# Optimization experiments

Hardware: AMD Instinct MI355X
Metric: run time of the kernel (lower is better)

Reference implementation:

```python
import jax, jax.numpy as jnp
import numpy as np

B, N, E = 2, 2048, 1024
H = 16
D = E // H  # head_dim = 64
MLP = 4096
EPS = 1e-5


def _layernorm(x, g, b):
    mu = jnp.mean(x, axis=-1, keepdims=True)
    var = jnp.var(x, axis=-1, keepdims=True)
    return (x - mu) * jax.lax.rsqrt(var + EPS) * g + b


def setup_inputs() -> dict:
    key = jax.random.key(0)
    ks = jax.random.split(key, 12)
    s_e = 1.0 / np.sqrt(E)
    s_m = 1.0 / np.sqrt(MLP)
    return {
        "x": jax.random.normal(ks[0], (B, N, E), jnp.float32),
        "w_qkv": jax.random.uniform(ks[1], (E, 3 * E), jnp.float32, -s_e, s_e),
        "b_qkv": jax.random.uniform(ks[2], (3 * E,), jnp.float32, -s_e, s_e),
        "w_proj": jax.random.uniform(ks[3], (E, E), jnp.float32, -s_e, s_e),
        "b_proj": jax.random.uniform(ks[4], (E,), jnp.float32, -s_e, s_e),
        "g1": jnp.ones((E,), jnp.float32),
        "beta1": jnp.zeros((E,), jnp.float32),
        "g2": jnp.ones((E,), jnp.float32),
        "beta2": jnp.zeros((E,), jnp.float32),
        "w_fc1": jax.random.uniform(ks[5], (E, MLP), jnp.float32, -s_e, s_e),
        "b_fc1": jax.random.uniform(ks[6], (MLP,), jnp.float32, -s_e, s_e),
        "w_fc2": jax.random.uniform(ks[7], (MLP, E), jnp.float32, -s_m, s_m),
        "b_fc2": jax.random.uniform(ks[8], (E,), jnp.float32, -s_m, s_m),
    }


def reference(x, w_qkv, b_qkv, w_proj, b_proj, g1, beta1, g2, beta2,
              w_fc1, b_fc1, w_fc2, b_fc2):
    scale = D ** (-0.5)
    # --- attention block (pre-norm) ---
    h = _layernorm(x, g1, beta1)
    qkv = (h @ w_qkv + b_qkv).reshape(B, N, 3, H, D)
    q, k, v = (qkv[:, :, i].transpose(0, 2, 1, 3) for i in range(3))  # [B,H,N,D]
    scores = jnp.einsum("bhnd,bhmd->bhnm", q, k) * scale  # [B,H,N,N]
    attn = jax.nn.softmax(scores, axis=-1)
    out = jnp.einsum("bhnm,bhmd->bhnd", attn, v)
    out = out.transpose(0, 2, 1, 3).reshape(B, N, E)
    x = x + (out @ w_proj + b_proj)
    # --- MLP block (pre-norm, exact GELU as in torch default) ---
    h = _layernorm(x, g2, beta2)
    h = jax.nn.gelu(h @ w_fc1 + b_fc1, approximate=False) @ w_fc2 + b_fc2
    return x + h
```

## Files before the change

### kernel.cpp

```cpp
#include <hip/hip_runtime.h>
#include <hip/hip_bf16.h>
#include <cmath>


typedef __hip_bfloat16 bf16;
typedef __bf16 bf16x8 __attribute__((ext_vector_type(8)));
typedef __bf16 bf16x4v __attribute__((ext_vector_type(4)));
typedef float  f32x4  __attribute__((ext_vector_type(4)));

#define CB 2
#define CN 2048
#define CE 1024
#define CH 16
#define CD 64
#define CMLP 4096
#define CM (CB*CN)

#define PS2 72

#define QPRE 0.18033688011112042f
#if __has_builtin(__builtin_amdgcn_exp2f)
#define EXP2(s) __builtin_amdgcn_exp2f(s)
#else
#define EXP2(s) __expf((s)*0.69314718055994531f)
#endif

__device__ __forceinline__ float b2f(bf16 v){ return __bfloat162float(v); }
__device__ __forceinline__ bf16  f2b(float v){ return __float2bfloat16(v); }

__device__ __forceinline__ void gl_lds16(const void* g, void* l){
  __builtin_amdgcn_global_load_lds((__attribute__((address_space(1))) void*)g,
                                   (__attribute__((address_space(3))) void*)l,
                                   16, 0, 0);
}

#define FENCE asm volatile("" ::: "memory")
#define BAR   do{ FENCE; __builtin_amdgcn_s_barrier(); FENCE; }while(0)
#define VMW6  asm volatile("s_waitcnt vmcnt(6)" ::: "memory")
#define VMW0  asm volatile("s_waitcnt vmcnt(0)" ::: "memory")

__global__ __launch_bounds__(256) void prep_k(
  const float* __restrict__ i0, bf16* __restrict__ o0,
  const float* __restrict__ i1, bf16* __restrict__ o1,
  const float* __restrict__ i2, bf16* __restrict__ o2,
  const float* __restrict__ i3, bf16* __restrict__ o3,
  const float* __restrict__ x,  const float* __restrict__ g,
  const float* __restrict__ be, bf16* __restrict__ lnout)
{
  __shared__ float tile[32][33];
  __shared__ float red[8];
  __shared__ float mu_s, rs_s;
  int t = blockIdx.x;
  const int tid = threadIdx.x;
  if(t >= 12288){
    const int row = t - 12288;
    const float4 v4 = ((const float4*)(x + (size_t)row*CE))[tid];
    float v[4] = {v4.x, v4.y, v4.z, v4.w};
    float s=0.f, s2=0.f;
    #pragma unroll
    for(int i=0;i<4;i++){ s+=v[i]; s2+=v[i]*v[i]; }
    #pragma unroll
    for(int off=32; off>0; off>>=1){ s += __shfl_down(s,off); s2 += __shfl_down(s2,off); }
    const int wv=tid>>6, ln=tid&63;
    if(ln==0){ red[wv]=s; red[4+wv]=s2; }
    __syncthreads();
    if(tid==0){
      float S=red[0]+red[1]+red[2]+red[3], S2=red[4]+red[5]+red[6]+red[7];
      float mu=S/CE;
      mu_s=mu; rs_s=rsqrtf(S2/CE - mu*mu + 1e-5f);
    }
    __syncthreads();
    const float mu=mu_s, rs=rs_s;
    #pragma unroll
    for(int i=0;i<4;i++){
      int c=tid*4+i;
      lnout[(size_t)row*CE+c] = f2b((v[i]-mu)*rs*g[c] + be[c]);
    }
    return;
  }
  const float* in; bf16* out; int K, N, nx;
  if(t < 3072){            in=i0; out=o0; K=1024; N=3072; nx=96; }
  else if(t < 4096){ t-=3072; in=i1; out=o1; K=1024; N=1024; nx=32; }
  else if(t < 8192){ t-=4096; in=i2; out=o2; K=1024; N=4096; nx=128; }
  else {             t-=8192; in=i3; out=o3; K=4096; N=1024; nx=32; }
  const int n0 = (t%nx)*32, k0 = (t/nx)*32;
  const int tx = tid & 31;
  const int ty = tid >> 5;
  #pragma unroll
  for(int i=0;i<32;i+=8) tile[ty+i][tx] = in[(size_t)(k0+ty+i)*N + n0+tx];
  __syncthreads();
  #pragma unroll
  for(int i=0;i<32;i+=8) out[(size_t)(n0+ty+i)*K + k0+tx] = f2b(tile[tx][ty+i]);
}

__global__ __launch_bounds__(256) void ln_k(const float* __restrict__ x,
                                            const float* __restrict__ g,
                                            const float* __restrict__ be,
                                            bf16* __restrict__ out){
  const int row = blockIdx.x;
  const int t = threadIdx.x;
  const float4 v4 = ((const float4*)(x + (size_t)row*CE))[t];
  float v[4] = {v4.x, v4.y, v4.z, v4.w};
  float s=0.f, s2=0.f;
  #pragma unroll
  for(int i=0;i<4;i++){ s+=v[i]; s2+=v[i]*v[i]; }
  #pragma unroll
  for(int off=32; off>0; off>>=1){ s += __shfl_down(s,off); s2 += __shfl_down(s2,off); }
  __shared__ float red[8];
  __shared__ float mu_s, rs_s;
  const int wv=t>>6, ln=t&63;
  if(ln==0){ red[wv]=s; red[4+wv]=s2; }
  __syncthreads();
  if(t==0){
    float S=red[0]+red[1]+red[2]+red[3], S2=red[4]+red[5]+red[6]+red[7];
    float mu=S/CE;
    mu_s=mu; rs_s=rsqrtf(S2/CE - mu*mu + 1e-5f);
  }
  __syncthreads();
  const float mu=mu_s, rs=rs_s;
  #pragma unroll
  for(int i=0;i<4;i++){
    int c=t*4+i;
    out[(size_t)row*CE+c] = f2b((v[i]-mu)*rs*g[c] + be[c]);
  }
}

#define EP_QKV 0
#define EP_RES 1
#define EP_GELU 2

template<int MODE, int BN>
__global__ __launch_bounds__(256,2) void gemm_k(
  const bf16* __restrict__ A, const bf16* __restrict__ BT,
  const float* __restrict__ bias, const float* __restrict__ res,
  float* __restrict__ Cf, bf16* __restrict__ Cb,
  bf16* __restrict__ Cq, bf16* __restrict__ Ck, bf16* __restrict__ Cv,
  int Ksz, int Nsz)
{
  constexpr int NJ = BN/32;
  constexpr int NBUF = (BN==64) ? 3 : 2;
  __shared__ __align__(16) bf16 Alds[NBUF][128*64];
  __shared__ __align__(16) bf16 Blds[NBUF][BN*64];
  const int tid = threadIdx.x;
  const int wave = tid>>6, lane = tid&63;
  const int m16 = lane&15, quad = lane>>4;
  const int wi = wave>>1, wj = wave&1;

  const int lin = blockIdx.x + gridDim.x*blockIdx.y;
  const int m_idx = (lin&7) + 8*((lin>>3)&3);
  const int n_idx = lin>>5;
  const size_t m0 = (size_t)m_idx*128;
  const size_t n0 = (size_t)n_idx*BN;

  f32x4 acc[4][NJ] = {};

  const int srow8 = lane>>3;
  const int schk  = ((lane&7)^srow8)*8;
  const bf16* pA = A  + (m0 + 32*wave      + srow8)*(size_t)Ksz + schk;
  const bf16* pB = BT + (n0 + (BN/4)*wave  + srow8)*(size_t)Ksz + schk;

  auto stage = [&](int buf, const bf16* gA, const bf16* gB){
    bf16* lA = &Alds[buf][wave*2048];
    bf16* lB = &Blds[buf][wave*(BN*16)];
    #pragma unroll
    for(int j=0;j<4;j++)  gl_lds16(gA + (size_t)(j*8)*Ksz, lA + j*512);
    #pragma unroll
    for(int j=0;j<NJ;j++) gl_lds16(gB + (size_t)(j*8)*Ksz, lB + j*512);
  };
  auto compute = [&](int buf){
    #pragma unroll
    for(int w=0;w<2;w++){
      const int sw = (m16&7);
      bf16x8 af[4], bfr[NJ];
      #pragma unroll
      for(int i=0;i<4;i++){
        const int row = wi*64+16*i+m16;
        af[i] = *(const bf16x8*)(&Alds[buf][row*64 + ((w*4+quad)^sw)*8]);
      }
      #pragma unroll
      for(int j=0;j<NJ;j++){
        const int row = wj*(BN/2)+16*j+m16;
        bfr[j] = *(const bf16x8*)(&Blds[buf][row*64 + ((w*4+quad)^sw)*8]);
      }
      #pragma unroll
      for(int i=0;i<4;i++)
        #pragma unroll
        for(int j=0;j<NJ;j++)
          acc[i][j] = __builtin_amdgcn_mfma_f32_16x16x32_bf16(af[i], bfr[j], acc[i][j], 0,0,0);
    }
  };

  const int kIters = Ksz/64;
  if constexpr (BN==64){
    stage(0, pA, pB); pA += 64; pB += 64;
    stage(1, pA, pB); pA += 64; pB += 64;
    int bc = 0, bs = 2;
    for(int kb=0; kb<kIters; ++kb){
      if(kb==kIters-1){ VMW0; } else { VMW6; }
      BAR;
      if(kb+2<kIters){ stage(bs, pA, pB); pA += 64; pB += 64; }
      compute(bc);
      bc = (bc==2)?0:bc+1;
      bs = (bs==2)?0:bs+1;
    }
  } else {
    stage(0, pA, pB); pA += 64; pB += 64;
    for(int kb=0; kb<kIters; ++kb){
      __syncthreads();
      if(kb+1<kIters){ stage((kb+1)&1, pA, pB); pA += 64; pB += 64; }
      compute(kb&1);
    }
  }

  #pragma unroll
  for(int i=0;i<4;i++){
    #pragma unroll
    for(int j=0;j<NJ;j++){
      const int col = (int)n0 + wj*(BN/2) + 16*j + m16;
      const float bcol = bias[col];
      #pragma unroll
      for(int r=0;r<4;r++){
        const int row = (int)m0 + wi*64 + 16*i + quad*4 + r;
        float v = acc[i][j][r] + bcol;
        if constexpr (MODE==EP_QKV){
          const int b = row>>11, n = row&2047;
          const int which = col>>10, cc = col&1023;
          const int h = cc>>6, d = cc&63;
          if(which==0)      Cq[(((size_t)(b*CH+h))*CN+n)*CD + d] = f2b(v*QPRE);
          else if(which==1) Ck[(((size_t)(b*CH+h))*CN+n)*CD + d] = f2b(v);
          else              Cv[(((size_t)(b*CH+h))*CD+d)*CN + n] = f2b(v);
        } else if constexpr (MODE==EP_RES){
          v += res[(size_t)row*Nsz+col];
          Cf[(size_t)row*Nsz+col] = v;
        } else {
          const float u2 = 1.5957691216f*(v + 0.044715f*v*v*v);
          v = v * (1.f/(1.f + __expf(-u2)));
          Cb[(size_t)row*Nsz+col] = f2b(v);
        }
      }
    }
  }
}

__global__ __launch_bounds__(256,2) void attn_k(
  const bf16* __restrict__ Q, const bf16* __restrict__ Kx,
  const bf16* __restrict__ Vt, bf16* __restrict__ O)
{
  const int lin = blockIdx.x + gridDim.x*blockIdx.y;
  const int bh = (lin&7) + 8*(lin>>7);
  const int qblk = (lin>>3)&15;
  const int b = bh>>4, h = bh&15;
  const int tid = threadIdx.x;
  const int wave = tid>>6, lane = tid&63;
  const int m16 = lane&15, quad = lane>>4;
  const int sw = m16&7;
  const int q0 = qblk*128 + wave*32;

  const bf16* Qb = Q  + (size_t)bh*CN*CD;
  const bf16* Kb = Kx + (size_t)bh*CN*CD;
  const bf16* Vb = Vt + (size_t)bh*CD*CN;

  bf16x8 qf[2][2];
  #pragma unroll
  for(int g=0;g<2;g++){
    const bf16* qp = Qb + (size_t)(q0+g*16+m16)*CD + quad*8;
    qf[g][0] = *(const bf16x8*)(qp);
    qf[g][1] = *(const bf16x8*)(qp + 32);
  }

  bf16x8 onesv;
  #pragma unroll
  for(int i=0;i<8;i++) onesv[i] = (__bf16)1.0f;

  f32x4 lacc[2] = {};
  f32x4 oacc[2][4] = {};

  __shared__ __align__(16) bf16 Klds[2][64*64];
  __shared__ __align__(16) bf16 Vlds[2][64*64];
  __shared__ __align__(16) bf16 Plds[4][32*PS2];
  bf16* Pw = &Plds[wave][0];

  const int srow8 = lane>>3;
  const int kchk  = (lane&7) ^ srow8;
  const bf16* pK = Kb + (size_t)(wave*16 + srow8)*CD + kchk*8;
  const bf16* pV = Vb + (size_t)(wave*16 + srow8)*CN + kchk*8;
  const int ldso = wave*1024;

  auto stage = [&](int buf, int kt){
    #pragma unroll
    for(int j=0;j<2;j++){
      gl_lds16(pK + ((size_t)kt + (size_t)j*8)*CD, &Klds[buf][ldso + j*512]);
      gl_lds16(pV + (size_t)j*8*CN + kt,           &Vlds[buf][ldso + j*512]);
    }
  };

  stage(0, 0);
  const int nT = CN/64;
  for(int t=0; t<nT; ++t){
    __syncthreads();
    if(t+1<nT) stage((t+1)&1, (t+1)*64);
    const bf16* Kl = &Klds[t&1][0];
    const bf16* Vl = &Vlds[t&1][0];

    f32x4 sf0[4], sf1[4];
    #pragma unroll
    for(int f=0;f<4;f++){
      const bf16* kb = Kl + (f*16+m16)*64;
      bf16x8 k0 = *(const bf16x8*)(kb + ((quad   ^ sw)*8));
      bf16x8 k1 = *(const bf16x8*)(kb + (((quad+4)^ sw)*8));
      f32x4 t0 = {}, t1 = {};
      t0 = __builtin_amdgcn_mfma_f32_16x16x32_bf16(k0, qf[0][0], t0, 0,0,0);
      t0 = __builtin_amdgcn_mfma_f32_16x16x32_bf16(k1, qf[0][1], t0, 0,0,0);
      t1 = __builtin_amdgcn_mfma_f32_16x16x32_bf16(k0, qf[1][0], t1, 0,0,0);
      t1 = __builtin_amdgcn_mfma_f32_16x16x32_bf16(k1, qf[1][1], t1, 0,0,0);
      sf0[f]=t0; sf1[f]=t1;
    }
    #pragma unroll
    for(int f=0;f<4;f++){
      bf16x4v p0, p1;
      #pragma unroll
      for(int r=0;r<4;r++){
        p0[r] = (__bf16)EXP2(sf0[f][r]);
        p1[r] = (__bf16)EXP2(sf1[f][r]);
      }
      *(bf16x4v*)(Pw + (size_t)m16*PS2      + f*16 + quad*4) = p0;
      *(bf16x4v*)(Pw + (size_t)(16+m16)*PS2 + f*16 + quad*4) = p1;
    }
    asm volatile("s_waitcnt lgkmcnt(0)" ::: "memory");
    #pragma unroll
    for(int c=0;c<2;c++){
      const bf16x8 ap0 = *(const bf16x8*)(Pw + (size_t)m16*PS2      + c*32 + quad*8);
      const bf16x8 ap1 = *(const bf16x8*)(Pw + (size_t)(16+m16)*PS2 + c*32 + quad*8);
      lacc[0] = __builtin_amdgcn_mfma_f32_16x16x32_bf16(ap0, onesv, lacc[0], 0,0,0);
      lacc[1] = __builtin_amdgcn_mfma_f32_16x16x32_bf16(ap1, onesv, lacc[1], 0,0,0);
      #pragma unroll
      for(int dt=0;dt<4;dt++){
        const int d = dt*16+m16;
        bf16x8 bv = *(const bf16x8*)(Vl + d*64 + (((c*4+quad) ^ sw)*8));
        oacc[0][dt] = __builtin_amdgcn_mfma_f32_16x16x32_bf16(ap0, bv, oacc[0][dt], 0,0,0);
        oacc[1][dt] = __builtin_amdgcn_mfma_f32_16x16x32_bf16(ap1, bv, oacc[1][dt], 0,0,0);
      }
    }
  }
  #pragma unroll
  for(int g=0;g<2;g++){
    float linv[4];
    #pragma unroll
    for(int r=0;r<4;r++) linv[r] = 1.f / lacc[g][r];
    #pragma unroll
    for(int dt=0;dt<4;dt++){
      #pragma unroll
      for(int r=0;r<4;r++){
        const int row = q0 + g*16 + quad*4 + r;
        O[((size_t)(b*CN+row))*CE + h*CD + dt*16 + m16] = f2b(oacc[g][dt][r]*linv[r]);
      }
    }
  }
}

extern "C" void kernel_launch(void* const* d_in, const int* in_sizes, int n_in,
                              void* d_out, int out_size, void* d_ws, size_t ws_size,
                              hipStream_t stream)
{
  (void)in_sizes; (void)n_in; (void)out_size; (void)ws_size;
  const float* x     = (const float*)d_in[0];
  const float* w_qkv = (const float*)d_in[1];
  const float* b_qkv = (const float*)d_in[2];
  const float* w_proj= (const float*)d_in[3];
  const float* b_proj= (const float*)d_in[4];
  const float* g1    = (const float*)d_in[5];
  const float* be1   = (const float*)d_in[6];
  const float* g2    = (const float*)d_in[7];
  const float* be2   = (const float*)d_in[8];
  const float* w_fc1 = (const float*)d_in[9];
  const float* b_fc1 = (const float*)d_in[10];
  const float* w_fc2 = (const float*)d_in[11];
  const float* b_fc2 = (const float*)d_in[12];
  float* out = (float*)d_out;

  char* ws = (char*)d_ws;
  size_t off = 0;
  auto alloc = [&](size_t bytes)->char*{
    char* p = ws + off;
    off += (bytes + 255) & ~(size_t)255;
    return p;
  };
  bf16* wqkvT = (bf16*)alloc((size_t)3072*1024*2);
  bf16* wprojT= (bf16*)alloc((size_t)1024*1024*2);
  bf16* wfc1T = (bf16*)alloc((size_t)4096*1024*2);
  bf16* wfc2T = (bf16*)alloc((size_t)1024*4096*2);
  bf16* h1    = (bf16*)alloc((size_t)CM*CE*2);
  bf16* q     = (bf16*)alloc((size_t)CM*CE*2);
  bf16* kk    = (bf16*)alloc((size_t)CM*CE*2);
  bf16* vT    = (bf16*)alloc((size_t)CM*CE*2);
  bf16* aO    = (bf16*)alloc((size_t)CM*CE*2);
  float* x2   = (float*)alloc((size_t)CM*CE*4);
  bf16* hmlp  = q;

  prep_k<<<12288+CM,256,0,stream>>>(w_qkv, wqkvT, w_proj, wprojT,
                                    w_fc1, wfc1T, w_fc2, wfc2T,
                                    x, g1, be1, h1);

  gemm_k<EP_QKV,128><<<dim3(3072/128, CM/128),256,0,stream>>>(
      h1, wqkvT, b_qkv, nullptr, nullptr, nullptr, q, kk, vT, 1024, 3072);
  attn_k<<<dim3(CN/128, CB*CH),256,0,stream>>>(q, kk, vT, aO);
  gemm_k<EP_RES,64><<<dim3(1024/64, CM/128),256,0,stream>>>(
      aO, wprojT, b_proj, x, x2, nullptr, nullptr,nullptr,nullptr, 1024, 1024);
  ln_k<<<CM,256,0,stream>>>(x2, g2, be2, h1);
  gemm_k<EP_GELU,128><<<dim3(4096/128, CM/128),256,0,stream>>>(
      h1, wfc1T, b_fc1, nullptr, nullptr, hmlp, nullptr,nullptr,nullptr, 1024, 4096);
  gemm_k<EP_RES,64><<<dim3(1024/64, CM/128),256,0,stream>>>(
      hmlp, wfc2T, b_fc2, x2, out, nullptr, nullptr,nullptr,nullptr, 4096, 1024);
}
```

Baseline: 333.8 us.

## Overlap remaining weight transposes with QKV GEMM in one fused launch

The prep kernel now transposes and converts only the QKV weight alongside LayerNorm 1. The proj, fc1 and fc2 weight transposes move into extra blocks of a new dedicated QKV GEMM kernel, so they run while the QKV GEMM tiles execute. The aim is to hide the transpose memory traffic behind the GEMM compute and shorten the prep stage on the critical path. The trade-off is that the transpose blocks compete with the GEMM blocks for bandwidth and CU slots, and they reserve the GEMM's large LDS allocation, which may cut occupancy for those blocks.

```diff
diff --git a/kernel.cpp b/kernel.cpp
--- a/kernel.cpp
+++ b/kernel.cpp
@@ -41,9 +41,6 @@
 
 __global__ __launch_bounds__(256) void prep_k(
   const float* __restrict__ i0, bf16* __restrict__ o0,
-  const float* __restrict__ i1, bf16* __restrict__ o1,
-  const float* __restrict__ i2, bf16* __restrict__ o2,
-  const float* __restrict__ i3, bf16* __restrict__ o3,
   const float* __restrict__ x,  const float* __restrict__ g,
   const float* __restrict__ be, bf16* __restrict__ lnout)
 {
@@ -52,8 +49,8 @@
   __shared__ float mu_s, rs_s;
   int t = blockIdx.x;
   const int tid = threadIdx.x;
-  if(t >= 12288){
-    const int row = t - 12288;
+  if(t >= 3072){
+    const int row = t - 3072;
     const float4 v4 = ((const float4*)(x + (size_t)row*CE))[tid];
     float v[4] = {v4.x, v4.y, v4.z, v4.w};
     float s=0.f, s2=0.f;
@@ -78,19 +75,14 @@
     }
     return;
   }
-  const float* in; bf16* out; int K, N, nx;
-  if(t < 3072){            in=i0; out=o0; K=1024; N=3072; nx=96; }
-  else if(t < 4096){ t-=3072; in=i1; out=o1; K=1024; N=1024; nx=32; }
-  else if(t < 8192){ t-=4096; in=i2; out=o2; K=1024; N=4096; nx=128; }
-  else {             t-=8192; in=i3; out=o3; K=4096; N=1024; nx=32; }
-  const int n0 = (t%nx)*32, k0 = (t/nx)*32;
+  const int n0 = (t%96)*32, k0 = (t/96)*32;
   const int tx = tid & 31;
   const int ty = tid >> 5;
   #pragma unroll
-  for(int i=0;i<32;i+=8) tile[ty+i][tx] = in[(size_t)(k0+ty+i)*N + n0+tx];
+  for(int i=0;i<32;i+=8) tile[ty+i][tx] = i0[(size_t)(k0+ty+i)*3072 + n0+tx];
   __syncthreads();
   #pragma unroll
-  for(int i=0;i<32;i+=8) out[(size_t)(n0+ty+i)*K + k0+tx] = f2b(tile[tx][ty+i]);
+  for(int i=0;i<32;i+=8) o0[(size_t)(n0+ty+i)*1024 + k0+tx] = f2b(tile[tx][ty+i]);
 }
 
 __global__ __launch_bounds__(256) void ln_k(const float* __restrict__ x,
@@ -129,12 +121,121 @@
 #define EP_RES 1
 #define EP_GELU 2
 
+__global__ __launch_bounds__(256,2) void qkvt_k(
+  const bf16* __restrict__ A, const bf16* __restrict__ BT,
+  const float* __restrict__ bias,
+  bf16* __restrict__ Cq, bf16* __restrict__ Ck, bf16* __restrict__ Cv,
+  const float* __restrict__ i1, bf16* __restrict__ o1,
+  const float* __restrict__ i2, bf16* __restrict__ o2,
+  const float* __restrict__ i3, bf16* __restrict__ o3)
+{
+  __shared__ __align__(16) bf16 Alds[2][128*64];
+  __shared__ __align__(16) bf16 Blds[2][128*64];
+  const int tid = threadIdx.x;
+
+  if(blockIdx.x >= 768){
+    float (*tile)[33] = (float(*)[33])(&Alds[0][0]);
+    int t = blockIdx.x - 768;
+    const float* in; bf16* out; int K, N, nx;
+    if(t < 1024){            in=i1; out=o1; K=1024; N=1024; nx=32; }
+    else if(t < 5120){ t-=1024; in=i2; out=o2; K=1024; N=4096; nx=128; }
+    else {             t-=5120; in=i3; out=o3; K=4096; N=1024; nx=32; }
+    const int n0 = (t%nx)*32, k0 = (t/nx)*32;
+    const int tx = tid & 31;
+    const int ty = tid >> 5;
+    #pragma unroll
+    for(int i=0;i<32;i+=8) tile[ty+i][tx] = in[(size_t)(k0+ty+i)*N + n0+tx];
+    __syncthreads();
+    #pragma unroll
+    for(int i=0;i<32;i+=8) out[(size_t)(n0+ty+i)*K + k0+tx] = f2b(tile[tx][ty+i]);
+    return;
+  }
+
+  constexpr int BN = 128;
+  constexpr int NJ = 4;
+  const int Ksz = 1024;
+  const int wave = tid>>6, lane = tid&63;
+  const int m16 = lane&15, quad = lane>>4;
+  const int wi = wave>>1, wj = wave&1;
+
+  const int lin = blockIdx.x;
+  const int m_idx = (lin&7) + 8*((lin>>3)&3);
+  const int n_idx = lin>>5;
+  const size_t m0 = (size_t)m_idx*128;
+  const size_t n0 = (size_t)n_idx*BN;
+
+  f32x4 acc[4][NJ] = {};
+
+  const int srow8 = lane>>3;
+  const int schk  = ((lane&7)^srow8)*8;
+  const bf16* pA = A  + (m0 + 32*wave      + srow8)*(size_t)Ksz + schk;
+  const bf16* pB = BT + (n0 + (BN/4)*wave  + srow8)*(size_t)Ksz + schk;
+
+  auto stage = [&](int buf, const bf16* gA, const bf16* gB){
+    bf16* lA = &Alds[buf][wave*2048];
+    bf16* lB = &Blds[buf][wave*(BN*16)];
+    #pragma unroll
+    for(int j=0;j<4;j++)  gl_lds16(gA + (size_t)(j*8)*Ksz, lA + j*512);
+    #pragma unroll
+    for(int j=0;j<NJ;j++) gl_lds16(gB + (size_t)(j*8)*Ksz, lB + j*512);
+  };
+  auto compute = [&](int buf){
+    #pragma unroll
+    for(int w=0;w<2;w++){
+      const int sw = (m16&7);
+      bf16x8 af[4], bfr[NJ];
+      #pragma unroll
+      for(int i=0;i<4;i++){
+        const int row = wi*64+16*i+m16;
+        af[i] = *(const bf16x8*)(&Alds[buf][row*64 + ((w*4+quad)^sw)*8]);
+      }
+      #pragma unroll
+      for(int j=0;j<NJ;j++){
+        const int row = wj*(BN/2)+16*j+m16;
+        bfr[j] = *(const bf16x8*)(&Blds[buf][row*64 + ((w*4+quad)^sw)*8]);
+      }
+      #pragma unroll
+      for(int i=0;i<4;i++)
+        #pragma unroll
+        for(int j=0;j<NJ;j++)
+          acc[i][j] = __builtin_amdgcn_mfma_f32_16x16x32_bf16(af[i], bfr[j], acc[i][j], 0,0,0);
+    }
+  };
+
+  const int kIters = Ksz/64;
+  stage(0, pA, pB); pA += 64; pB += 64;
+  for(int kb=0; kb<kIters; ++kb){
+    __syncthreads();
+    if(kb+1<kIters){ stage((kb+1)&1, pA, pB); pA += 64; pB += 64; }
+    compute(kb&1);
+  }
+
+  #pragma unroll
+  for(int i=0;i<4;i++){
+    #pragma unroll
+    for(int j=0;j<NJ;j++){
+      const int col = (int)n0 + wj*(BN/2) + 16*j + m16;
+      const float bcol = bias[col];
+      #pragma unroll
+      for(int r=0;r<4;r++){
+        const int row = (int)m0 + wi*64 + 16*i + quad*4 + r;
+        float v = acc[i][j][r] + bcol;
+        const int b = row>>11, n = row&2047;
+        const int which = col>>10, cc = col&1023;
+        const int h = cc>>6, d = cc&63;
+        if(which==0)      Cq[(((size_t)(b*CH+h))*CN+n)*CD + d] = f2b(v*QPRE);
+        else if(which==1) Ck[(((size_t)(b*CH+h))*CN+n)*CD + d] = f2b(v);
+        else              Cv[(((size_t)(b*CH+h))*CD+d)*CN + n] = f2b(v);
+      }
+    }
+  }
+}
+
 template<int MODE, int BN>
 __global__ __launch_bounds__(256,2) void gemm_k(
   const bf16* __restrict__ A, const bf16* __restrict__ BT,
   const float* __restrict__ bias, const float* __restrict__ res,
   float* __restrict__ Cf, bf16* __restrict__ Cb,
-  bf16* __restrict__ Cq, bf16* __restrict__ Ck, bf16* __restrict__ Cv,
   int Ksz, int Nsz)
 {
   constexpr int NJ = BN/32;
@@ -222,14 +323,7 @@
       for(int r=0;r<4;r++){
         const int row = (int)m0 + wi*64 + 16*i + quad*4 + r;
         float v = acc[i][j][r] + bcol;
-        if constexpr (MODE==EP_QKV){
-          const int b = row>>11, n = row&2047;
-          const int which = col>>10, cc = col&1023;
-          const int h = cc>>6, d = cc&63;
-          if(which==0)      Cq[(((size_t)(b*CH+h))*CN+n)*CD + d] = f2b(v*QPRE);
-          else if(which==1) Ck[(((size_t)(b*CH+h))*CN+n)*CD + d] = f2b(v);
-          else              Cv[(((size_t)(b*CH+h))*CD+d)*CN + n] = f2b(v);
-        } else if constexpr (MODE==EP_RES){
+        if constexpr (MODE==EP_RES){
           v += res[(size_t)row*Nsz+col];
           Cf[(size_t)row*Nsz+col] = v;
         } else {
@@ -397,18 +491,17 @@
   float* x2   = (float*)alloc((size_t)CM*CE*4);
   bf16* hmlp  = q;
 
-  prep_k<<<12288+CM,256,0,stream>>>(w_qkv, wqkvT, w_proj, wprojT,
-                                    w_fc1, wfc1T, w_fc2, wfc2T,
-                                    x, g1, be1, h1);
-
-  gemm_k<EP_QKV,128><<<dim3(3072/128, CM/128),256,0,stream>>>(
-      h1, wqkvT, b_qkv, nullptr, nullptr, nullptr, q, kk, vT, 1024, 3072);
+  prep_k<<<3072+CM,256,0,stream>>>(w_qkv, wqkvT, x, g1, be1, h1);
+
+  qkvt_k<<<768+9216,256,0,stream>>>(h1, wqkvT, b_qkv, q, kk, vT,
+                                    w_proj, wprojT, w_fc1, wfc1T,
+                                    w_fc2, wfc2T);
   attn_k<<<dim3(CN/128, CB*CH),256,0,stream>>>(q, kk, vT, aO);
   gemm_k<EP_RES,64><<<dim3(1024/64, CM/128),256,0,stream>>>(
-      aO, wprojT, b_proj, x, x2, nullptr, nullptr,nullptr,nullptr, 1024, 1024);
+      aO, wprojT, b_proj, x, x2, nullptr, 1024, 1024);
   ln_k<<<CM,256,0,stream>>>(x2, g2, be2, h1);
   gemm_k<EP_GELU,128><<<dim3(4096/128, CM/128),256,0,stream>>>(
-      h1, wfc1T, b_fc1, nullptr, nullptr, hmlp, nullptr,nullptr,nullptr, 1024, 4096);
+      h1, wfc1T, b_fc1, nullptr, nullptr, hmlp, 1024, 4096);
   gemm_k<EP_RES,64><<<dim3(1024/64, CM/128),256,0,stream>>>(
-      hmlp, wfc2T, b_fc2, x2, out, nullptr, nullptr,nullptr,nullptr, 4096, 1024);
-}
+      hmlp, wfc2T, b_fc2, x2, out, nullptr, 4096, 1024);
+}
```

Result: slower. 341.6 us (+2.3%).
